# Optimization experiments

Measured on AMD Instinct MI355X. Metric: run time of the kernel, lower is better.

Reference implementation:

```python
import jax, jax.numpy as jnp
import numpy as np

BATCH = 4096  # number of rows in the sparse input matrix (static for segment_sum)


def setup_inputs() -> dict:
    key = jax.random.key(0)
    k1, k2, k3, k4 = jax.random.split(key, 4)
    nnz = 262144
    in_features, out_features = 32000, 256
    row_idx = jnp.sort(jax.random.randint(k1, (nnz,), 0, BATCH, dtype=jnp.int32))
    col_idx = jax.random.randint(k2, (nnz,), 0, in_features, dtype=jnp.int32)
    vals = jax.random.uniform(k3, (nnz,), dtype=jnp.float32)
    weight = jax.random.normal(k4, (in_features, out_features), dtype=jnp.float32) / np.sqrt(out_features)
    bias = jnp.zeros((out_features,), dtype=jnp.float32)
    return {"row_idx": row_idx, "col_idx": col_idx, "vals": vals,
            "weight": weight, "bias": bias}


def reference(row_idx, col_idx, vals, weight, bias):
    # out = sparse_input @ weight + bias
    # sparse_input is COO: (row_idx, col_idx, vals), shape [BATCH, in_features]
    # gather weight rows for each nonzero, scale by value, sum per output row
    contrib = vals[:, None] * weight[col_idx]          # [nnz, out_features]
    out = jax.ops.segment_sum(contrib, row_idx, num_segments=BATCH)  # [BATCH, out]
    return out + bias
```

## Files before the change

### kernel.cpp

```cpp
#include <hip/hip_runtime.h>
#include <hip/hip_bf16.h>


constexpr int BATCH = 4096;

__device__ inline unsigned short f2bf(float f) {
    unsigned u = __float_as_uint(f);
    unsigned r = (u + 0x7FFFu + ((u >> 16) & 1u)) >> 16;
    return (unsigned short)r;
}

__global__ __launch_bounds__(256) void prep_kernel(
    const float* __restrict__ weight,
    unsigned short* __restrict__ wb,
    const int* __restrict__ row_idx, int nnz,
    int* __restrict__ ptr,
    int n_w4, int conv_blocks)
{
    if ((int)blockIdx.x < conv_blocks) {
        const int t = blockIdx.x * 256 + threadIdx.x;
        if (t < n_w4) {
            const float4 f = reinterpret_cast<const float4*>(weight)[t];
            ushort4 o;
            o.x = f2bf(f.x); o.y = f2bf(f.y); o.z = f2bf(f.z); o.w = f2bf(f.w);
            reinterpret_cast<ushort4*>(wb)[t] = o;
        }
    } else {
        const int i = (blockIdx.x - conv_blocks) * 256 + threadIdx.x;
        if (i >= nnz) return;
        const int r  = row_idx[i];
        const int rn = (i + 1 < nnz) ? row_idx[i + 1] : BATCH;
        for (int rr = r + 1; rr <= rn; ++rr) ptr[rr] = i + 1;
        if (i == 0)
            for (int rr = 0; rr <= r; ++rr) ptr[rr] = 0;
    }
}

__device__ inline void fma_bf(float v, uint2 w, float4& acc) {
    acc.x = fmaf(v, __uint_as_float(w.x << 16),          acc.x);
    acc.y = fmaf(v, __uint_as_float(w.x & 0xFFFF0000u), acc.y);
    acc.z = fmaf(v, __uint_as_float(w.y << 16),          acc.z);
    acc.w = fmaf(v, __uint_as_float(w.y & 0xFFFF0000u), acc.w);
}

__global__ __launch_bounds__(256, 8) void sparse_linear_bf16(
    const int*            __restrict__ col_idx,
    const float*          __restrict__ vals,
    const unsigned short* __restrict__ wb,
    const float*          __restrict__ bias,
    const int*            __restrict__ ptr,
    float*                __restrict__ out,
    int nnz)
{
    __shared__ float4 part[4][64];

    const int wave = threadIdx.x >> 6;
    const int lane = threadIdx.x & 63;
    const int rloc = wave >> 1;
    const int half = wave & 1;
    const int r    = blockIdx.x * 2 + rloc;

    const int start = ptr[r];
    const int end   = ptr[r + 1];
    const int chunk = (end - start + 1) >> 1;

    int k  = start + half * chunk;
    int ke = min(k + chunk, end);

    const uint2* __restrict__ W = reinterpret_cast<const uint2*>(wb);

    float4 acc = make_float4(0.f, 0.f, 0.f, 0.f);

    while (k + 8 <= ke) {
        const int kb = __builtin_amdgcn_readfirstlane(k);
        const int   c0 = col_idx[kb + 0], c1 = col_idx[kb + 1];
        const int   c2 = col_idx[kb + 2], c3 = col_idx[kb + 3];
        const int   c4 = col_idx[kb + 4], c5 = col_idx[kb + 5];
        const int   c6 = col_idx[kb + 6], c7 = col_idx[kb + 7];
        const float v0 = vals[kb + 0], v1 = vals[kb + 1];
        const float v2 = vals[kb + 2], v3 = vals[kb + 3];
        const float v4 = vals[kb + 4], v5 = vals[kb + 5];
        const float v6 = vals[kb + 6], v7 = vals[kb + 7];
        const uint2 w0 = W[(size_t)c0 * 64 + lane];
        const uint2 w1 = W[(size_t)c1 * 64 + lane];
        const uint2 w2 = W[(size_t)c2 * 64 + lane];
        const uint2 w3 = W[(size_t)c3 * 64 + lane];
        const uint2 w4 = W[(size_t)c4 * 64 + lane];
        const uint2 w5 = W[(size_t)c5 * 64 + lane];
        const uint2 w6 = W[(size_t)c6 * 64 + lane];
        const uint2 w7 = W[(size_t)c7 * 64 + lane];
        fma_bf(v0, w0, acc); fma_bf(v1, w1, acc);
        fma_bf(v2, w2, acc); fma_bf(v3, w3, acc);
        fma_bf(v4, w4, acc); fma_bf(v5, w5, acc);
        fma_bf(v6, w6, acc); fma_bf(v7, w7, acc);
        k += 8;
    }

    const int rem = ke - k;
    if (rem > 0) {
        const int kb = __builtin_amdgcn_readfirstlane(k);
        #pragma unroll
        for (int j = 0; j < 8; ++j) {
            const int   kk = min(kb + j, nnz - 1);
            const int   c  = col_idx[kk];
            const float v  = (j < rem) ? vals[kk] : 0.0f;
            const uint2 w  = W[(size_t)c * 64 + lane];
            fma_bf(v, w, acc);
        }
    }

    part[wave][lane] = acc;
    __syncthreads();

    if (threadIdx.x < 128) {
        const int rl = threadIdx.x >> 6;
        const int ln = threadIdx.x & 63;
        const float4 p0 = part[2 * rl + 0][ln];
        const float4 p1 = part[2 * rl + 1][ln];
        const float4 b  = reinterpret_cast<const float4*>(bias)[ln];
        float4 o;
        o.x = (p0.x + p1.x) + b.x;
        o.y = (p0.y + p1.y) + b.y;
        o.z = (p0.z + p1.z) + b.z;
        o.w = (p0.w + p1.w) + b.w;
        reinterpret_cast<float4*>(out)[(size_t)(blockIdx.x * 2 + rl) * 64 + ln] = o;
    }
}

extern "C" void kernel_launch(void* const* d_in, const int* in_sizes, int n_in,
                              void* d_out, int out_size, void* d_ws, size_t ws_size,
                              hipStream_t stream)
{
    const int*   row_idx = (const int*)  d_in[0];
    const int*   col_idx = (const int*)  d_in[1];
    const float* vals    = (const float*)d_in[2];
    const float* weight  = (const float*)d_in[3];
    const float* bias    = (const float*)d_in[4];
    float*       out     = (float*)      d_out;
    const int    nnz     = in_sizes[0];
    const int    w_elems = in_sizes[3];

    unsigned short* wb      = (unsigned short*)d_ws;
    int*            row_ptr = (int*)((char*)d_ws + (32u << 20));

    const int n_w4        = w_elems / 4;
    const int conv_blocks = (n_w4 + 255) / 256;
    const int rptr_blocks = (nnz + 255) / 256;

    hipLaunchKernelGGL(prep_kernel, dim3(conv_blocks + rptr_blocks), dim3(256), 0, stream,
                       weight, wb, row_idx, nnz, row_ptr, n_w4, conv_blocks);
    hipLaunchKernelGGL(sparse_linear_bf16, dim3(BATCH / 2), dim3(256), 0, stream,
                       col_idx, vals, wb, bias, row_ptr, out, nnz);
}
```

Before: 105.1 us.

## Slice bf16 weight into column blocks and split SpMM across eight slices

The prep kernel now writes the bf16 weight in a sliced layout, 8 column slices of 32 outputs each, stored contiguously per slice. The SpMM kernel launches 8 blocks per group of 4 rows, one per slice. Each wave handles 4 nonzeros at once with 16 lanes per nonzero reading 64-byte weight rows, then reduces across lanes with shuffles. The aim is a smaller per-block working set in cache and more parallelism, replacing the shared-memory split. In exchange, col_idx and vals are re-read 8 times and each gather is narrower.

Result: slower. 110.0 us (+4.6%).

```diff
diff --git a/kernel.cpp b/kernel.cpp
--- a/kernel.cpp
+++ b/kernel.cpp
@@ -1,5 +1,4 @@
 #include <hip/hip_runtime.h>
-#include <hip/hip_bf16.h>
 
 
 constexpr int BATCH = 4096;
@@ -15,15 +14,19 @@
     unsigned short* __restrict__ wb,
     const int* __restrict__ row_idx, int nnz,
     int* __restrict__ ptr,
-    int n_w4, int conv_blocks)
+    int in_f, int conv_blocks)
 {
     if ((int)blockIdx.x < conv_blocks) {
-        const int t = blockIdx.x * 256 + threadIdx.x;
-        if (t < n_w4) {
-            const float4 f = reinterpret_cast<const float4*>(weight)[t];
+        const int wave = threadIdx.x >> 6;
+        const int lane = threadIdx.x & 63;
+        const int r    = blockIdx.x * 4 + wave;
+        if (r < in_f) {
+            const float4 f = reinterpret_cast<const float4*>(weight)[r * 64 + lane];
             ushort4 o;
             o.x = f2bf(f.x); o.y = f2bf(f.y); o.z = f2bf(f.z); o.w = f2bf(f.w);
-            reinterpret_cast<ushort4*>(wb)[t] = o;
+            const int slice = lane >> 3;
+            const size_t idx4 = ((size_t)slice * in_f + r) * 8 + (lane & 7);
+            reinterpret_cast<ushort4*>(wb)[idx4] = o;
         }
     } else {
         const int i = (blockIdx.x - conv_blocks) * 256 + threadIdx.x;
@@ -36,94 +39,60 @@
     }
 }
 
-__device__ inline void fma_bf(float v, uint2 w, float4& acc) {
-    acc.x = fmaf(v, __uint_as_float(w.x << 16),          acc.x);
-    acc.y = fmaf(v, __uint_as_float(w.x & 0xFFFF0000u), acc.y);
-    acc.z = fmaf(v, __uint_as_float(w.y << 16),          acc.z);
-    acc.w = fmaf(v, __uint_as_float(w.y & 0xFFFF0000u), acc.w);
-}
-
-__global__ __launch_bounds__(256, 8) void sparse_linear_bf16(
+__global__ __launch_bounds__(256, 8) void spmm_sliced(
     const int*            __restrict__ col_idx,
     const float*          __restrict__ vals,
     const unsigned short* __restrict__ wb,
     const float*          __restrict__ bias,
     const int*            __restrict__ ptr,
     float*                __restrict__ out,
-    int nnz)
+    int nnz, int in_f)
 {
-    __shared__ float4 part[4][64];
-
-    const int wave = threadIdx.x >> 6;
-    const int lane = threadIdx.x & 63;
-    const int rloc = wave >> 1;
-    const int half = wave & 1;
-    const int r    = blockIdx.x * 2 + rloc;
+    const int wave  = threadIdx.x >> 6;
+    const int lane  = threadIdx.x & 63;
+    const int slice = blockIdx.x & 7;
+    const int r     = (blockIdx.x >> 3) * 4 + wave;
 
     const int start = ptr[r];
     const int end   = ptr[r + 1];
-    const int chunk = (end - start + 1) >> 1;
 
-    int k  = start + half * chunk;
-    int ke = min(k + chunk, end);
+    const int j    = lane >> 4;
+    const int cpos = lane & 15;
 
-    const uint2* __restrict__ W = reinterpret_cast<const uint2*>(wb);
+    const unsigned* __restrict__ Ws =
+        reinterpret_cast<const unsigned*>(wb) + (size_t)slice * in_f * 16;
 
-    float4 acc = make_float4(0.f, 0.f, 0.f, 0.f);
+    float ax = 0.f, ay = 0.f;
 
-    while (k + 8 <= ke) {
-        const int kb = __builtin_amdgcn_readfirstlane(k);
-        const int   c0 = col_idx[kb + 0], c1 = col_idx[kb + 1];
-        const int   c2 = col_idx[kb + 2], c3 = col_idx[kb + 3];
-        const int   c4 = col_idx[kb + 4], c5 = col_idx[kb + 5];
-        const int   c6 = col_idx[kb + 6], c7 = col_idx[kb + 7];
-        const float v0 = vals[kb + 0], v1 = vals[kb + 1];
-        const float v2 = vals[kb + 2], v3 = vals[kb + 3];
-        const float v4 = vals[kb + 4], v5 = vals[kb + 5];
-        const float v6 = vals[kb + 6], v7 = vals[kb + 7];
-        const uint2 w0 = W[(size_t)c0 * 64 + lane];
-        const uint2 w1 = W[(size_t)c1 * 64 + lane];
-        const uint2 w2 = W[(size_t)c2 * 64 + lane];
-        const uint2 w3 = W[(size_t)c3 * 64 + lane];
-        const uint2 w4 = W[(size_t)c4 * 64 + lane];
-        const uint2 w5 = W[(size_t)c5 * 64 + lane];
-        const uint2 w6 = W[(size_t)c6 * 64 + lane];
-        const uint2 w7 = W[(size_t)c7 * 64 + lane];
-        fma_bf(v0, w0, acc); fma_bf(v1, w1, acc);
-        fma_bf(v2, w2, acc); fma_bf(v3, w3, acc);
-        fma_bf(v4, w4, acc); fma_bf(v5, w5, acc);
-        fma_bf(v6, w6, acc); fma_bf(v7, w7, acc);
-        k += 8;
+    int k = start;
+    for (; k + 16 <= end; k += 16) {
+        #pragma unroll
+        for (int t = 0; t < 4; ++t) {
+            const int   kk = k + t * 4 + j;
+            const int   c  = col_idx[kk];
+            const float v  = vals[kk];
+            const unsigned w = Ws[(size_t)c * 16 + cpos];
+            ax = fmaf(v, __uint_as_float(w << 16),          ax);
+            ay = fmaf(v, __uint_as_float(w & 0xFFFF0000u), ay);
+        }
+    }
+    for (; k < end; k += 4) {
+        const int   kk    = k + j;
+        const bool  valid = kk < end;
+        const int   c     = col_idx[valid ? kk : (nnz - 1)];
+        const float v     = valid ? vals[kk] : 0.0f;
+        const unsigned w  = Ws[(size_t)c * 16 + cpos];
+        ax = fmaf(v, __uint_as_float(w << 16),          ax);
+        ay = fmaf(v, __uint_as_float(w & 0xFFFF0000u), ay);
     }
 
-    const int rem = ke - k;
-    if (rem > 0) {
-        const int kb = __builtin_amdgcn_readfirstlane(k);
-        #pragma unroll
-        for (int j = 0; j < 8; ++j) {
-            const int   kk = min(kb + j, nnz - 1);
-            const int   c  = col_idx[kk];
-            const float v  = (j < rem) ? vals[kk] : 0.0f;
-            const uint2 w  = W[(size_t)c * 64 + lane];
-            fma_bf(v, w, acc);
-        }
-    }
+    ax += __shfl_xor(ax, 16); ax += __shfl_xor(ax, 32);
+    ay += __shfl_xor(ay, 16); ay += __shfl_xor(ay, 32);
 
-    part[wave][lane] = acc;
-    __syncthreads();
-
-    if (threadIdx.x < 128) {
-        const int rl = threadIdx.x >> 6;
-        const int ln = threadIdx.x & 63;
-        const float4 p0 = part[2 * rl + 0][ln];
-        const float4 p1 = part[2 * rl + 1][ln];
-        const float4 b  = reinterpret_cast<const float4*>(bias)[ln];
-        float4 o;
-        o.x = (p0.x + p1.x) + b.x;
-        o.y = (p0.y + p1.y) + b.y;
-        o.z = (p0.z + p1.z) + b.z;
-        o.w = (p0.w + p1.w) + b.w;
-        reinterpret_cast<float4*>(out)[(size_t)(blockIdx.x * 2 + rl) * 64 + ln] = o;
+    if (lane < 16) {
+        const float2 b = reinterpret_cast<const float2*>(bias)[slice * 16 + cpos];
+        float2 o; o.x = ax + b.x; o.y = ay + b.y;
+        reinterpret_cast<float2*>(out)[(size_t)r * 128 + slice * 16 + cpos] = o;
     }
 }
 
@@ -138,17 +107,16 @@
     const float* bias    = (const float*)d_in[4];
     float*       out     = (float*)      d_out;
     const int    nnz     = in_sizes[0];
-    const int    w_elems = in_sizes[3];
+    const int    in_f    = in_sizes[3] / 256;
 
     unsigned short* wb      = (unsigned short*)d_ws;
     int*            row_ptr = (int*)((char*)d_ws + (32u << 20));
 
-    const int n_w4        = w_elems / 4;
-    const int conv_blocks = (n_w4 + 255) / 256;
+    const int conv_blocks = (in_f + 3) / 4;
     const int rptr_blocks = (nnz + 255) / 256;
 
     hipLaunchKernelGGL(prep_kernel, dim3(conv_blocks + rptr_blocks), dim3(256), 0, stream,
-                       weight, wb, row_idx, nnz, row_ptr, n_w4, conv_blocks);
-    hipLaunchKernelGGL(sparse_linear_bf16, dim3(BATCH / 2), dim3(256), 0, stream,
-                       col_idx, vals, wb, bias, row_ptr, out, nnz);
+                       weight, wb, row_idx, nnz, row_ptr, in_f, conv_blocks);
+    hipLaunchKernelGGL(spmm_sliced, dim3((BATCH / 4) * 8), dim3(256), 0, stream,
+                       col_idx, vals, wb, bias, row_ptr, out, nnz, in_f);
 }
```
